# Performance work log

Hardware: AMD Instinct MI355X
Metric: run time of the kernel (lower is better)

## Reference

```python
import jax, jax.numpy as jnp
import numpy as np

B, T, D = 2, 2048, 1024
NH = 16
HD = D // NH


def setup_inputs() -> dict:
    key = jax.random.key(0)
    ks = jax.random.split(key, 5)
    s = 0.02
    return {
        "x": jax.random.normal(ks[0], (B, T, D), dtype=jnp.float32),
        "Wq": jax.random.normal(ks[1], (D, D), dtype=jnp.float32) * s,
        "Wk": jax.random.normal(ks[2], (D, D), dtype=jnp.float32) * s,
        "Wv": jax.random.normal(ks[3], (D, D), dtype=jnp.float32) * s,
        "Wo": jax.random.normal(ks[4], (D, D), dtype=jnp.float32) * s,
        "bo": jnp.zeros((D,), dtype=jnp.float32),
    }


def reference(x, Wq, Wk, Wv, Wo, bo):
    b, t, _ = x.shape
    scale = HD ** -0.5
    # torch Linear: y = x @ W^T
    q = (x @ Wq.T).reshape(b, t, NH, HD)
    k = (x @ Wk.T).reshape(b, t, NH, HD)
    v = (x @ Wv.T).reshape(b, t, NH, HD)
    # scores: [b, nh, t, t]
    s = jnp.einsum("bqhd,bkhd->bhqk", q, k) * scale
    causal = jnp.tril(jnp.ones((t, t), dtype=bool))
    s = jnp.where(causal, s, -jnp.inf)
    p = jax.nn.softmax(s, axis=-1)
    o = jnp.einsum("bhqk,bkhd->bqhd", p, v).reshape(b, t, D)
    return o @ Wo.T + bo
```

## Files before the change

kernel.cpp:

```cpp
#include <hip/hip_runtime.h>


typedef __bf16 bf16x8 __attribute__((ext_vector_type(8)));
typedef float f32x4 __attribute__((ext_vector_type(4)));
typedef unsigned short ushortx8 __attribute__((ext_vector_type(8)));
typedef unsigned short ushortx4 __attribute__((ext_vector_type(4)));

#define T_SEQ 2048
#define NHEAD 16
#define HDIM 64
#define DMODEL 1024

__device__ inline unsigned short f2bf(float f) {
  unsigned int u = __builtin_bit_cast(unsigned int, f);
  unsigned int r = (u + 0x7fffu + ((u >> 16) & 1u)) >> 16;
  return (unsigned short)r;
}

__device__ inline void gl16(const unsigned short* g, unsigned short* l) {
  __builtin_amdgcn_global_load_lds(
      (const __attribute__((address_space(1))) unsigned int*)g,
      (__attribute__((address_space(3))) unsigned int*)l, 16, 0, 0);
}

__global__ void cast_all(const float* __restrict__ x, const float* __restrict__ w0,
                         const float* __restrict__ w1, const float* __restrict__ w2,
                         const float* __restrict__ w3, unsigned short* __restrict__ out) {
  const int NX = 2 * T_SEQ * DMODEL;
  int i = (blockIdx.x * 256 + threadIdx.x) * 4;
  const float* src;
  int off;
  if (i < NX) {
    src = x; off = i;
  } else {
    const int j = i - NX;
    const int sel = j >> 20;
    off = j & ((1 << 20) - 1);
    src = sel == 0 ? w0 : sel == 1 ? w1 : sel == 2 ? w2 : w3;
  }
  float4 v = *reinterpret_cast<const float4*>(src + off);
  ushortx4 o;
  o[0] = f2bf(v.x); o[1] = f2bf(v.y); o[2] = f2bf(v.z); o[3] = f2bf(v.w);
  *reinterpret_cast<ushortx4*>(out + i) = o;
}

__device__ __forceinline__ void gemm_core(
    const unsigned short* __restrict__ A, const unsigned short* __restrict__ Bw,
    int K, int m0, int n0, f32x4 acc[4][4]) {
  __shared__ unsigned short As[4096];
  __shared__ unsigned short Bs[4096];
  const int tid = threadIdx.x;
  const int lane = tid & 63, wid = tid >> 6;
  const int wr = wid >> 1, wc = wid & 1;
  const int lr = lane & 15, lg = lane >> 4;
  const int srow = tid >> 2;
  const int scs = ((tid & 3) ^ (srow & 3)) * 8;
  const unsigned short* ga0 = A + (size_t)(m0 + srow) * K + scs;
  const unsigned short* gb0 = Bw + (size_t)(n0 + srow) * K + scs;
  unsigned short* la0 = As + tid * 8;
  unsigned short* lb0 = Bs + tid * 8;
  const int rca = (lg ^ (lr & 3)) * 8;

  for (int k0 = 0; k0 < K; k0 += 32) {
    __syncthreads();
    gl16(ga0 + k0, la0);
    gl16(ga0 + (size_t)64 * K + k0, la0 + 2048);
    gl16(gb0 + k0, lb0);
    gl16(gb0 + (size_t)64 * K + k0, lb0 + 2048);
    __syncthreads();

    bf16x8 af[4], bfr[4];
#pragma unroll
    for (int t = 0; t < 4; ++t) {
      af[t]  = *reinterpret_cast<const bf16x8*>(&As[(wr * 64 + t * 16 + lr) * 32 + rca]);
      bfr[t] = *reinterpret_cast<const bf16x8*>(&Bs[(wc * 64 + t * 16 + lr) * 32 + rca]);
    }
#pragma unroll
    for (int mi = 0; mi < 4; ++mi)
#pragma unroll
      for (int ni = 0; ni < 4; ++ni)
        acc[mi][ni] = __builtin_amdgcn_mfma_f32_16x16x32_bf16(af[mi], bfr[ni], acc[mi][ni], 0, 0, 0);
  }
}

__device__ __forceinline__ void gemm_core_n64(
    const unsigned short* __restrict__ A, const unsigned short* __restrict__ Bw,
    int K, int m0, int n0, f32x4 acc[4][2]) {
  __shared__ unsigned short As[4096];
  __shared__ unsigned short Bs[2048];
  const int tid = threadIdx.x;
  const int lane = tid & 63, wid = tid >> 6;
  const int wr = wid >> 1, wc = wid & 1;
  const int lr = lane & 15, lg = lane >> 4;
  const int srow = tid >> 2;
  const int scs = ((tid & 3) ^ (srow & 3)) * 8;
  const unsigned short* ga0 = A + (size_t)(m0 + srow) * K + scs;
  const unsigned short* gb0 = Bw + (size_t)(n0 + srow) * K + scs;
  unsigned short* la0 = As + tid * 8;
  unsigned short* lb0 = Bs + tid * 8;
  const int rca = (lg ^ (lr & 3)) * 8;

  for (int k0 = 0; k0 < K; k0 += 32) {
    __syncthreads();
    gl16(ga0 + k0, la0);
    gl16(ga0 + (size_t)64 * K + k0, la0 + 2048);
    gl16(gb0 + k0, lb0);
    __syncthreads();

    bf16x8 af[4], bfr[2];
#pragma unroll
    for (int t = 0; t < 4; ++t)
      af[t] = *reinterpret_cast<const bf16x8*>(&As[(wr * 64 + t * 16 + lr) * 32 + rca]);
#pragma unroll
    for (int t = 0; t < 2; ++t)
      bfr[t] = *reinterpret_cast<const bf16x8*>(&Bs[(wc * 32 + t * 16 + lr) * 32 + rca]);
#pragma unroll
    for (int mi = 0; mi < 4; ++mi)
#pragma unroll
      for (int ni = 0; ni < 2; ++ni)
        acc[mi][ni] = __builtin_amdgcn_mfma_f32_16x16x32_bf16(af[mi], bfr[ni], acc[mi][ni], 0, 0, 0);
  }
}

__global__ __launch_bounds__(256) void gemm_qkv(
    const unsigned short* __restrict__ xb, const unsigned short* __restrict__ Wall,
    unsigned short* __restrict__ Qb, unsigned short* __restrict__ Kb,
    unsigned short* __restrict__ Vtb) {
  const int z = blockIdx.y;
  const int bid = blockIdx.x;
  int m0, n0;
  const unsigned short* A;
  const unsigned short* Bw;
  if (z < 2) {
    n0 = (bid & 7) * 128; m0 = (bid >> 3) * 128;
    A = xb; Bw = Wall + (size_t)z * (DMODEL * DMODEL);
  } else {
    m0 = (bid & 7) * 128; n0 = (bid >> 3) * 128;
    A = Wall + (size_t)2 * (DMODEL * DMODEL); Bw = xb;
  }
  f32x4 acc[4][4] = {};
  gemm_core(A, Bw, DMODEL, m0, n0, acc);

  const int tid = threadIdx.x, lane = tid & 63, wid = tid >> 6;
  const int wr = wid >> 1, wc = wid & 1, lr = lane & 15, lg = lane >> 4;
  const int mb = m0 + wr * 64, nb = n0 + wc * 64;
  const float scale = z == 0 ? 0.125f * 1.44269504089f : 1.0f;
#pragma unroll
  for (int mi = 0; mi < 4; ++mi)
#pragma unroll
    for (int ni = 0; ni < 4; ++ni) {
      const int col = nb + ni * 16 + lr;
#pragma unroll
      for (int j = 0; j < 4; ++j) {
        const int row = mb + mi * 16 + lg * 4 + j;
        const float v = acc[mi][ni][j] * scale;
        if (z < 2) {
          const int b = row >> 11, t = row & (T_SEQ - 1);
          const int h = col >> 6, d = col & (HDIM - 1);
          unsigned short* out = z == 0 ? Qb : Kb;
          out[(((size_t)(b * NHEAD + h) * T_SEQ + t) << 6) + d] = f2bf(v);
        } else {
          const int h = row >> 6, d = row & (HDIM - 1);
          const int b = col >> 11, tt = col & (T_SEQ - 1);
          const int nib = (tt >> 2) & 7;
          const int nib2 = ((nib & 3) << 1) | (nib >> 2);
          const int tp = (tt & ~31) | (nib2 << 2) | (tt & 3);
          Vtb[(((size_t)(b * NHEAD + h) * HDIM + d) << 11) + tp] = f2bf(v);
        }
      }
    }
}

__global__ __launch_bounds__(256) void gemm_proj(
    const unsigned short* __restrict__ Ob, const unsigned short* __restrict__ Wob,
    float* __restrict__ out, const float* __restrict__ bias) {
  const int m0 = blockIdx.y * 128, n0 = blockIdx.x * 64;
  f32x4 acc[4][2] = {};
  gemm_core_n64(Ob, Wob, DMODEL, m0, n0, acc);

  const int tid = threadIdx.x, lane = tid & 63, wid = tid >> 6;
  const int wr = wid >> 1, wc = wid & 1, lr = lane & 15, lg = lane >> 4;
  const int mb = m0 + wr * 64, nb = n0 + wc * 32;
#pragma unroll
  for (int mi = 0; mi < 4; ++mi)
#pragma unroll
    for (int ni = 0; ni < 2; ++ni) {
      const int col = nb + ni * 16 + lr;
      const float bv = bias[col];
#pragma unroll
      for (int j = 0; j < 4; ++j) {
        const int row = mb + mi * 16 + lg * 4 + j;
        out[(size_t)row * DMODEL + col] = acc[mi][ni][j] + bv;
      }
    }
}

__device__ __forceinline__ void attn_step(
    const unsigned short* Kslot, const unsigned short* Vslot,
    const int kh0, const int kh1, const int (&vo)[2],
    const bf16x8 (&qf)[2], f32x4 (&acc)[4], float& mrun, float& lrun,
    const bool domask, const int kb, const int q, const int lg) {
  f32x4 s[4] = {};
  __builtin_amdgcn_s_setprio(1);
#pragma unroll
  for (int c = 0; c < 4; ++c) {
    bf16x8 k0 = *reinterpret_cast<const bf16x8*>(&Kslot[kh0 + c * 1024]);
    bf16x8 k1 = *reinterpret_cast<const bf16x8*>(&Kslot[kh1 + c * 1024]);
    s[c] = __builtin_amdgcn_mfma_f32_16x16x32_bf16(k0, qf[0], s[c], 0, 0, 0);
    s[c] = __builtin_amdgcn_mfma_f32_16x16x32_bf16(k1, qf[1], s[c], 0, 0, 0);
  }
  __builtin_amdgcn_s_setprio(0);
  if (domask) {
#pragma unroll
    for (int c = 0; c < 4; ++c)
#pragma unroll
      for (int j = 0; j < 4; ++j) {
        const int k = kb + c * 16 + lg * 4 + j;
        if (k > q) s[c][j] = -INFINITY;
      }
  }
  float tm = -INFINITY;
#pragma unroll
  for (int c = 0; c < 4; ++c)
#pragma unroll
    for (int j = 0; j < 4; ++j) tm = fmaxf(tm, s[c][j]);
  tm = fmaxf(tm, __shfl_xor(tm, 16, 64));
  tm = fmaxf(tm, __shfl_xor(tm, 32, 64));
  if (!__all(tm <= mrun + 8.f)) {
    const float mnew = fmaxf(mrun, tm);
    const float fac = exp2f(mrun - mnew);
    lrun *= fac;
#pragma unroll
    for (int dt = 0; dt < 4; ++dt)
#pragma unroll
      for (int j = 0; j < 4; ++j) acc[dt][j] *= fac;
    mrun = mnew;
  }
  float tsum = 0.f;
#pragma unroll
  for (int c = 0; c < 4; ++c)
#pragma unroll
    for (int j = 0; j < 4; ++j) {
      const float p = exp2f(s[c][j] - mrun);
      s[c][j] = p;
      tsum += p;
    }
  lrun += tsum;

  bf16x8 pb[2];
#pragma unroll
  for (int ks = 0; ks < 2; ++ks) {
    bf16x8 t8;
#pragma unroll
    for (int e = 0; e < 8; ++e) t8[e] = (__bf16)s[ks * 2 + (e >> 2)][e & 3];
    pb[ks] = t8;
  }
  __builtin_amdgcn_s_setprio(1);
#pragma unroll
  for (int dt = 0; dt < 4; ++dt) {
#pragma unroll
    for (int ks = 0; ks < 2; ++ks) {
      bf16x8 vf = *reinterpret_cast<const bf16x8*>(&Vslot[vo[ks] + dt * 1024]);
      acc[dt] = __builtin_amdgcn_mfma_f32_16x16x32_bf16(vf, pb[ks], acc[dt], 0, 0, 0);
    }
  }
  __builtin_amdgcn_s_setprio(0);
}

__global__ __launch_bounds__(512, 4) void flash_attn(
    const unsigned short* __restrict__ Q, const unsigned short* __restrict__ Kg,
    const unsigned short* __restrict__ Vt, unsigned short* __restrict__ O) {
  __shared__ unsigned short Ks[5][4096];
  __shared__ unsigned short Vs[5][4096];
  const int tid = threadIdx.x, lane = tid & 63, wid = tid >> 6;
  const int lr = lane & 15, lg = lane >> 4, wq = wid & 3;
  const int bid = blockIdx.x;
  const int bh = (bid & 7) * 4 + ((bid >> 3) & 3);
  const int a = (bid >> 5) & 15;
  const int b = 31 - a;
  const bool g0 = wid < 4;
  const int myq1 = g0 ? a : b;
  const int q1 = myq1 * 64 + wq * 16 + lr;
  const int q2 = b * 64 + wq * 16 + lr;
  const size_t base = (size_t)bh * (T_SEQ * HDIM);

  bf16x8 qf1[2], qf2[2];
#pragma unroll
  for (int h = 0; h < 2; ++h) {
    qf1[h] = *reinterpret_cast<const bf16x8*>(Q + base + (size_t)q1 * HDIM + h * 32 + lg * 8);
    qf2[h] = *reinterpret_cast<const bf16x8*>(Q + base + (size_t)q2 * HDIM + h * 32 + lg * 8);
  }

  const int srow = tid >> 3;
  const int schk = ((tid & 7) ^ (srow & 7)) * 8;
  const unsigned short* kst = Kg + base + (size_t)srow * HDIM + schk;
  const unsigned short* vst = Vt + base + (size_t)srow * T_SEQ + schk;

#define STAGE(slot, kt_)                                \
  do {                                                  \
    const int kb_ = (kt_) * 64;                         \
    gl16(kst + (size_t)kb_ * HDIM, &Ks[slot][tid * 8]); \
    gl16(vst + kb_, &Vs[slot][tid * 8]);                \
  } while (0)

  const int kh0 = lr * 64 + ((lg ^ (lr & 7)) * 8);
  const int kh1 = lr * 64 + (((4 + lg) ^ (lr & 7)) * 8);
  int vo[2];
#pragma unroll
  for (int ks = 0; ks < 2; ++ks)
    vo[ks] = lr * 64 + (((ks * 4 + lg) ^ (lr & 7)) * 8);

  float m1 = -INFINITY, l1 = 0.f, m2 = -INFINITY, l2 = 0.f;
  f32x4 acc1[4] = {}, acc2[4] = {};

  STAGE(0, 0);
  STAGE(1, 1);
  asm volatile("s_waitcnt vmcnt(2)" ::: "memory");
  __builtin_amdgcn_s_barrier();
  asm volatile("" ::: "memory");

  int sl = 0;
  for (int kt = 0; kt <= a; ++kt) {
    const int st = kt + 2;
    int sst = sl + 2; if (sst >= 5) sst -= 5;
    if (st <= b) STAGE(sst, st);
    attn_step(Ks[sl], Vs[sl], kh0, kh1, vo, qf1, acc1, m1, l1,
              g0 && (kt == a), kt * 64, q1, lg);
    if (kt < a && st <= b) {
      asm volatile("s_waitcnt vmcnt(2)" ::: "memory");
    } else {
      asm volatile("s_waitcnt vmcnt(0)" ::: "memory");
    }
    __builtin_amdgcn_s_barrier();
    asm volatile("" ::: "memory");
    ++sl; if (sl >= 5) sl -= 5;
  }

  {
    int s3 = sl + 2; if (s3 >= 5) s3 -= 5;
    if (a + 3 <= b) STAGE(s3, a + 3);
  }
  for (int t0 = a + 1; t0 <= b; t0 += 2) {
    int s1 = sl + 1; if (s1 >= 5) s1 -= 5;
    int s3 = sl + 3; if (s3 >= 5) s3 -= 5;
    int s4 = sl + 4; if (s4 >= 5) s4 -= 5;
    if (t0 + 3 <= b) STAGE(s3, t0 + 3);
    if (t0 + 4 <= b) STAGE(s4, t0 + 4);
    if (!g0) {
      attn_step(Ks[sl], Vs[sl], kh0, kh1, vo, qf2, acc1, m1, l1,
                t0 == b, t0 * 64, q2, lg);
    } else if (t0 + 1 <= b) {
      attn_step(Ks[s1], Vs[s1], kh0, kh1, vo, qf2, acc2, m2, l2,
                false, (t0 + 1) * 64, q2, lg);
    }
    if (t0 + 4 <= b) {
      asm volatile("s_waitcnt vmcnt(2)" ::: "memory");
    } else {
      asm volatile("s_waitcnt vmcnt(0)" ::: "memory");
    }
    __builtin_amdgcn_s_barrier();
    asm volatile("" ::: "memory");
    sl += 2; if (sl >= 5) sl -= 5;
  }
#undef STAGE

  float* sm = reinterpret_cast<float*>(&Ks[0][0]);
  const int lid = (wq * 64 + lane) * 18;
  if (g0) {
    float* p = sm + lid;
    p[0] = m2; p[1] = l2;
#pragma unroll
    for (int dt = 0; dt < 4; ++dt)
#pragma unroll
      for (int j = 0; j < 4; ++j) p[2 + dt * 4 + j] = acc2[dt][j];
  }
  __syncthreads();
  if (!g0) {
    const float* p = sm + lid;
    const float mo = p[0], lo = p[1];
    const float ms = fmaxf(m1, mo);
    const float f1 = exp2f(m1 - ms), f2 = exp2f(mo - ms);
    l1 = l1 * f1 + lo * f2;
#pragma unroll
    for (int dt = 0; dt < 4; ++dt)
#pragma unroll
      for (int j = 0; j < 4; ++j)
        acc1[dt][j] = acc1[dt][j] * f1 + p[2 + dt * 4 + j] * f2;
  }

  l1 += __shfl_xor(l1, 16, 64);
  l1 += __shfl_xor(l1, 32, 64);

  const int b_ = bh >> 4, h_ = bh & (NHEAD - 1);
  const float inv = 1.0f / l1;
  unsigned short* orow = O + (((size_t)(b_ * T_SEQ + q1)) << 10) + h_ * HDIM + lg * 4;
#pragma unroll
  for (int dt = 0; dt < 4; ++dt) {
    ushortx4 o4;
#pragma unroll
    for (int j = 0; j < 4; ++j) o4[j] = f2bf(acc1[dt][j] * inv);
    *reinterpret_cast<ushortx4*>(orow + dt * 16) = o4;
  }
}

extern "C" void kernel_launch(void* const* d_in, const int* in_sizes, int n_in,
                              void* d_out, int out_size, void* d_ws, size_t ws_size,
                              hipStream_t stream) {
  const float* x  = (const float*)d_in[0];
  const float* Wq = (const float*)d_in[1];
  const float* Wk = (const float*)d_in[2];
  const float* Wv = (const float*)d_in[3];
  const float* Wo = (const float*)d_in[4];
  const float* bo = (const float*)d_in[5];
  float* out = (float*)d_out;

  const int M = 2 * T_SEQ;
  const int NXD = DMODEL * DMODEL;
  const int NX = M * DMODEL;

  unsigned short* ws = (unsigned short*)d_ws;
  unsigned short* xb  = ws;
  unsigned short* Wqb = xb + NX;
  unsigned short* Wob = Wqb + 3 * (size_t)NXD;
  unsigned short* Qb  = Wqb + 4 * (size_t)NXD;
  unsigned short* Kbf = Qb + NX;
  unsigned short* Vtb = Kbf + NX;
  unsigned short* Ob  = Vtb + NX;

  cast_all<<<(NX + 4 * NXD) / 1024, 256, 0, stream>>>(x, Wq, Wk, Wv, Wo, xb);

  dim3 gq(256, 3);
  gemm_qkv<<<gq, 256, 0, stream>>>(xb, Wqb, Qb, Kbf, Vtb);

  flash_attn<<<512, 512, 0, stream>>>(Qb, Kbf, Vtb, Ob);

  dim3 gg(DMODEL / 64, M / 128);
  gemm_proj<<<gg, 256, 0, stream>>>(Ob, Wob, out, bo);
}
```

Baseline: 104.1 us.

## Have each attention wave process both paired query tiles, sharing K/V fragment loads

The flash-attention block drops from 512 to 256 threads. Each wave now owns 16 rows of both the early query tile and its paired late query tile. During the shared causal prefix, one K/V fragment read from LDS feeds interleaved MFMAs for both query sets, and the tail is split into two independent accumulators that are merged in registers. This removes the end-of-kernel LDS exchange and __syncthreads, and halves LDS fragment reads per MFMA in the shared phase. The cost is higher register pressure, fewer waves per block, and each thread staging twice as many K/V chunks.

```diff
diff --git a/kernel.cpp b/kernel.cpp
--- a/kernel.cpp
+++ b/kernel.cpp
@@ -195,6 +195,44 @@
     }
 }
 
+__device__ __forceinline__ void softmax_pack(
+    f32x4 (&s)[4], f32x4 (&acc)[4], float& mrun, float& lrun, bf16x8 (&pb)[2]) {
+  float tm = -INFINITY;
+#pragma unroll
+  for (int c = 0; c < 4; ++c)
+#pragma unroll
+    for (int j = 0; j < 4; ++j) tm = fmaxf(tm, s[c][j]);
+  tm = fmaxf(tm, __shfl_xor(tm, 16, 64));
+  tm = fmaxf(tm, __shfl_xor(tm, 32, 64));
+  if (!__all(tm <= mrun + 8.f)) {
+    const float mnew = fmaxf(mrun, tm);
+    const float fac = exp2f(mrun - mnew);
+    lrun *= fac;
+#pragma unroll
+    for (int dt = 0; dt < 4; ++dt)
+#pragma unroll
+      for (int j = 0; j < 4; ++j) acc[dt][j] *= fac;
+    mrun = mnew;
+  }
+  float tsum = 0.f;
+#pragma unroll
+  for (int c = 0; c < 4; ++c)
+#pragma unroll
+    for (int j = 0; j < 4; ++j) {
+      const float p = exp2f(s[c][j] - mrun);
+      s[c][j] = p;
+      tsum += p;
+    }
+  lrun += tsum;
+#pragma unroll
+  for (int ks = 0; ks < 2; ++ks) {
+    bf16x8 t8;
+#pragma unroll
+    for (int e = 0; e < 8; ++e) t8[e] = (__bf16)s[ks * 2 + (e >> 2)][e & 3];
+    pb[ks] = t8;
+  }
+}
+
 __device__ __forceinline__ void attn_step(
     const unsigned short* Kslot, const unsigned short* Vslot,
     const int kh0, const int kh1, const int (&vo)[2],
@@ -219,76 +257,85 @@
         if (k > q) s[c][j] = -INFINITY;
       }
   }
-  float tm = -INFINITY;
-#pragma unroll
-  for (int c = 0; c < 4; ++c)
-#pragma unroll
-    for (int j = 0; j < 4; ++j) tm = fmaxf(tm, s[c][j]);
-  tm = fmaxf(tm, __shfl_xor(tm, 16, 64));
-  tm = fmaxf(tm, __shfl_xor(tm, 32, 64));
-  if (!__all(tm <= mrun + 8.f)) {
-    const float mnew = fmaxf(mrun, tm);
-    const float fac = exp2f(mrun - mnew);
-    lrun *= fac;
-#pragma unroll
-    for (int dt = 0; dt < 4; ++dt)
-#pragma unroll
-      for (int j = 0; j < 4; ++j) acc[dt][j] *= fac;
-    mrun = mnew;
-  }
-  float tsum = 0.f;
-#pragma unroll
-  for (int c = 0; c < 4; ++c)
-#pragma unroll
-    for (int j = 0; j < 4; ++j) {
-      const float p = exp2f(s[c][j] - mrun);
-      s[c][j] = p;
-      tsum += p;
-    }
-  lrun += tsum;
-
   bf16x8 pb[2];
-#pragma unroll
-  for (int ks = 0; ks < 2; ++ks) {
-    bf16x8 t8;
-#pragma unroll
-    for (int e = 0; e < 8; ++e) t8[e] = (__bf16)s[ks * 2 + (e >> 2)][e & 3];
-    pb[ks] = t8;
-  }
+  softmax_pack(s, acc, mrun, lrun, pb);
   __builtin_amdgcn_s_setprio(1);
 #pragma unroll
-  for (int dt = 0; dt < 4; ++dt) {
+  for (int dt = 0; dt < 4; ++dt)
 #pragma unroll
     for (int ks = 0; ks < 2; ++ks) {
       bf16x8 vf = *reinterpret_cast<const bf16x8*>(&Vslot[vo[ks] + dt * 1024]);
       acc[dt] = __builtin_amdgcn_mfma_f32_16x16x32_bf16(vf, pb[ks], acc[dt], 0, 0, 0);
     }
-  }
   __builtin_amdgcn_s_setprio(0);
 }
 
-__global__ __launch_bounds__(512, 4) void flash_attn(
+__device__ __forceinline__ void attn_step2(
+    const unsigned short* Kslot, const unsigned short* Vslot,
+    const int kh0, const int kh1, const int (&vo)[2],
+    const bf16x8 (&qfA)[2], f32x4 (&accA)[4], float& mA, float& lA, const bool maskA,
+    const bf16x8 (&qfB)[2], f32x4 (&accB)[4], float& mB, float& lB,
+    const int kb, const int qA, const int lg) {
+  bf16x8 kf[4][2];
+#pragma unroll
+  for (int c = 0; c < 4; ++c) {
+    kf[c][0] = *reinterpret_cast<const bf16x8*>(&Kslot[kh0 + c * 1024]);
+    kf[c][1] = *reinterpret_cast<const bf16x8*>(&Kslot[kh1 + c * 1024]);
+  }
+  f32x4 sA[4] = {}, sB[4] = {};
+  __builtin_amdgcn_s_setprio(1);
+#pragma unroll
+  for (int c = 0; c < 4; ++c) {
+    sA[c] = __builtin_amdgcn_mfma_f32_16x16x32_bf16(kf[c][0], qfA[0], sA[c], 0, 0, 0);
+    sB[c] = __builtin_amdgcn_mfma_f32_16x16x32_bf16(kf[c][0], qfB[0], sB[c], 0, 0, 0);
+    sA[c] = __builtin_amdgcn_mfma_f32_16x16x32_bf16(kf[c][1], qfA[1], sA[c], 0, 0, 0);
+    sB[c] = __builtin_amdgcn_mfma_f32_16x16x32_bf16(kf[c][1], qfB[1], sB[c], 0, 0, 0);
+  }
+  __builtin_amdgcn_s_setprio(0);
+  if (maskA) {
+#pragma unroll
+    for (int c = 0; c < 4; ++c)
+#pragma unroll
+      for (int j = 0; j < 4; ++j) {
+        const int k = kb + c * 16 + lg * 4 + j;
+        if (k > qA) sA[c][j] = -INFINITY;
+      }
+  }
+  bf16x8 pbA[2], pbB[2];
+  softmax_pack(sA, accA, mA, lA, pbA);
+  softmax_pack(sB, accB, mB, lB, pbB);
+  __builtin_amdgcn_s_setprio(1);
+#pragma unroll
+  for (int dt = 0; dt < 4; ++dt)
+#pragma unroll
+    for (int ks = 0; ks < 2; ++ks) {
+      bf16x8 vf = *reinterpret_cast<const bf16x8*>(&Vslot[vo[ks] + dt * 1024]);
+      accA[dt] = __builtin_amdgcn_mfma_f32_16x16x32_bf16(vf, pbA[ks], accA[dt], 0, 0, 0);
+      accB[dt] = __builtin_amdgcn_mfma_f32_16x16x32_bf16(vf, pbB[ks], accB[dt], 0, 0, 0);
+    }
+  __builtin_amdgcn_s_setprio(0);
+}
+
+__global__ __launch_bounds__(256, 2) void flash_attn(
     const unsigned short* __restrict__ Q, const unsigned short* __restrict__ Kg,
     const unsigned short* __restrict__ Vt, unsigned short* __restrict__ O) {
   __shared__ unsigned short Ks[5][4096];
   __shared__ unsigned short Vs[5][4096];
   const int tid = threadIdx.x, lane = tid & 63, wid = tid >> 6;
-  const int lr = lane & 15, lg = lane >> 4, wq = wid & 3;
+  const int lr = lane & 15, lg = lane >> 4;
   const int bid = blockIdx.x;
   const int bh = (bid & 7) * 4 + ((bid >> 3) & 3);
   const int a = (bid >> 5) & 15;
   const int b = 31 - a;
-  const bool g0 = wid < 4;
-  const int myq1 = g0 ? a : b;
-  const int q1 = myq1 * 64 + wq * 16 + lr;
-  const int q2 = b * 64 + wq * 16 + lr;
+  const int qA = a * 64 + wid * 16 + lr;
+  const int qB = b * 64 + wid * 16 + lr;
   const size_t base = (size_t)bh * (T_SEQ * HDIM);
 
-  bf16x8 qf1[2], qf2[2];
+  bf16x8 qfA[2], qfB[2];
 #pragma unroll
   for (int h = 0; h < 2; ++h) {
-    qf1[h] = *reinterpret_cast<const bf16x8*>(Q + base + (size_t)q1 * HDIM + h * 32 + lg * 8);
-    qf2[h] = *reinterpret_cast<const bf16x8*>(Q + base + (size_t)q2 * HDIM + h * 32 + lg * 8);
+    qfA[h] = *reinterpret_cast<const bf16x8*>(Q + base + (size_t)qA * HDIM + h * 32 + lg * 8);
+    qfB[h] = *reinterpret_cast<const bf16x8*>(Q + base + (size_t)qB * HDIM + h * 32 + lg * 8);
   }
 
   const int srow = tid >> 3;
@@ -296,11 +343,13 @@
   const unsigned short* kst = Kg + base + (size_t)srow * HDIM + schk;
   const unsigned short* vst = Vt + base + (size_t)srow * T_SEQ + schk;
 
-#define STAGE(slot, kt_)                                \
-  do {                                                  \
-    const int kb_ = (kt_) * 64;                         \
-    gl16(kst + (size_t)kb_ * HDIM, &Ks[slot][tid * 8]); \
-    gl16(vst + kb_, &Vs[slot][tid * 8]);                \
+#define STAGE(slot, kt_)                                              \
+  do {                                                                \
+    const int kb_ = (kt_) * 64;                                       \
+    gl16(kst + (size_t)kb_ * HDIM, &Ks[slot][tid * 8]);               \
+    gl16(kst + (size_t)(kb_ + 32) * HDIM, &Ks[slot][2048 + tid * 8]); \
+    gl16(vst + kb_, &Vs[slot][tid * 8]);                              \
+    gl16(vst + 32 * T_SEQ + kb_, &Vs[slot][2048 + tid * 8]);          \
   } while (0)
 
   const int kh0 = lr * 64 + ((lg ^ (lr & 7)) * 8);
@@ -310,24 +359,24 @@
   for (int ks = 0; ks < 2; ++ks)
     vo[ks] = lr * 64 + (((ks * 4 + lg) ^ (lr & 7)) * 8);
 
-  float m1 = -INFINITY, l1 = 0.f, m2 = -INFINITY, l2 = 0.f;
-  f32x4 acc1[4] = {}, acc2[4] = {};
+  float mA = -INFINITY, lA = 0.f, mB = -INFINITY, lB = 0.f;
+  f32x4 accA[4] = {}, accB[4] = {};
 
   STAGE(0, 0);
   STAGE(1, 1);
-  asm volatile("s_waitcnt vmcnt(2)" ::: "memory");
+  asm volatile("s_waitcnt vmcnt(4)" ::: "memory");
   __builtin_amdgcn_s_barrier();
   asm volatile("" ::: "memory");
 
   int sl = 0;
   for (int kt = 0; kt <= a; ++kt) {
-    const int st = kt + 2;
     int sst = sl + 2; if (sst >= 5) sst -= 5;
-    if (st <= b) STAGE(sst, st);
-    attn_step(Ks[sl], Vs[sl], kh0, kh1, vo, qf1, acc1, m1, l1,
-              g0 && (kt == a), kt * 64, q1, lg);
-    if (kt < a && st <= b) {
-      asm volatile("s_waitcnt vmcnt(2)" ::: "memory");
+    if (kt + 2 <= b) STAGE(sst, kt + 2);
+    attn_step2(Ks[sl], Vs[sl], kh0, kh1, vo,
+               qfA, accA, mA, lA, (kt == a),
+               qfB, accB, mB, lB, kt * 64, qA, lg);
+    if (kt < a) {
+      asm volatile("s_waitcnt vmcnt(4)" ::: "memory");
     } else {
       asm volatile("s_waitcnt vmcnt(0)" ::: "memory");
     }
@@ -337,24 +386,24 @@
   }
 
   {
-    int s3 = sl + 2; if (s3 >= 5) s3 -= 5;
-    if (a + 3 <= b) STAGE(s3, a + 3);
-  }
+    int sp = sl + 2; if (sp >= 5) sp -= 5;
+    if (a + 3 <= b) STAGE(sp, a + 3);
+  }
+  float m2 = -INFINITY, l2 = 0.f;
+  f32x4 acc2[4] = {};
   for (int t0 = a + 1; t0 <= b; t0 += 2) {
     int s1 = sl + 1; if (s1 >= 5) s1 -= 5;
     int s3 = sl + 3; if (s3 >= 5) s3 -= 5;
     int s4 = sl + 4; if (s4 >= 5) s4 -= 5;
     if (t0 + 3 <= b) STAGE(s3, t0 + 3);
     if (t0 + 4 <= b) STAGE(s4, t0 + 4);
-    if (!g0) {
-      attn_step(Ks[sl], Vs[sl], kh0, kh1, vo, qf2, acc1, m1, l1,
-                t0 == b, t0 * 64, q2, lg);
-    } else if (t0 + 1 <= b) {
-      attn_step(Ks[s1], Vs[s1], kh0, kh1, vo, qf2, acc2, m2, l2,
-                false, (t0 + 1) * 64, q2, lg);
-    }
+    attn_step(Ks[sl], Vs[sl], kh0, kh1, vo, qfB, accB, mB, lB,
+              (t0 == b), t0 * 64, qB, lg);
+    if (t0 + 1 <= b)
+      attn_step(Ks[s1], Vs[s1], kh0, kh1, vo, qfB, acc2, m2, l2,
+                false, (t0 + 1) * 64, qB, lg);
     if (t0 + 4 <= b) {
-      asm volatile("s_waitcnt vmcnt(2)" ::: "memory");
+      asm volatile("s_waitcnt vmcnt(4)" ::: "memory");
     } else {
       asm volatile("s_waitcnt vmcnt(0)" ::: "memory");
     }
@@ -364,42 +413,36 @@
   }
 #undef STAGE
 
-  float* sm = reinterpret_cast<float*>(&Ks[0][0]);
-  const int lid = (wq * 64 + lane) * 18;
-  if (g0) {
-    float* p = sm + lid;
-    p[0] = m2; p[1] = l2;
+  {
+    const float ms = fmaxf(mB, m2);
+    const float f1 = exp2f(mB - ms), f2 = exp2f(m2 - ms);
+    lB = lB * f1 + l2 * f2;
 #pragma unroll
     for (int dt = 0; dt < 4; ++dt)
 #pragma unroll
-      for (int j = 0; j < 4; ++j) p[2 + dt * 4 + j] = acc2[dt][j];
-  }
-  __syncthreads();
-  if (!g0) {
-    const float* p = sm + lid;
-    const float mo = p[0], lo = p[1];
-    const float ms = fmaxf(m1, mo);
-    const float f1 = exp2f(m1 - ms), f2 = exp2f(mo - ms);
-    l1 = l1 * f1 + lo * f2;
-#pragma unroll
-    for (int dt = 0; dt < 4; ++dt)
-#pragma unroll
       for (int j = 0; j < 4; ++j)
-        acc1[dt][j] = acc1[dt][j] * f1 + p[2 + dt * 4 + j] * f2;
-  }
-
-  l1 += __shfl_xor(l1, 16, 64);
-  l1 += __shfl_xor(l1, 32, 64);
+        accB[dt][j] = accB[dt][j] * f1 + acc2[dt][j] * f2;
+  }
+
+  lA += __shfl_xor(lA, 16, 64);
+  lA += __shfl_xor(lA, 32, 64);
+  lB += __shfl_xor(lB, 16, 64);
+  lB += __shfl_xor(lB, 32, 64);
 
   const int b_ = bh >> 4, h_ = bh & (NHEAD - 1);
-  const float inv = 1.0f / l1;
-  unsigned short* orow = O + (((size_t)(b_ * T_SEQ + q1)) << 10) + h_ * HDIM + lg * 4;
+  const float invA = 1.0f / lA, invB = 1.0f / lB;
+  unsigned short* orowA = O + (((size_t)(b_ * T_SEQ + qA)) << 10) + h_ * HDIM + lg * 4;
+  unsigned short* orowB = O + (((size_t)(b_ * T_SEQ + qB)) << 10) + h_ * HDIM + lg * 4;
 #pragma unroll
   for (int dt = 0; dt < 4; ++dt) {
-    ushortx4 o4;
-#pragma unroll
-    for (int j = 0; j < 4; ++j) o4[j] = f2bf(acc1[dt][j] * inv);
-    *reinterpret_cast<ushortx4*>(orow + dt * 16) = o4;
+    ushortx4 oa, ob;
+#pragma unroll
+    for (int j = 0; j < 4; ++j) {
+      oa[j] = f2bf(accA[dt][j] * invA);
+      ob[j] = f2bf(accB[dt][j] * invB);
+    }
+    *reinterpret_cast<ushortx4*>(orowA + dt * 16) = oa;
+    *reinterpret_cast<ushortx4*>(orowB + dt * 16) = ob;
   }
 }
 
@@ -432,7 +475,7 @@
   dim3 gq(256, 3);
   gemm_qkv<<<gq, 256, 0, stream>>>(xb, Wqb, Qb, Kbf, Vtb);
 
-  flash_attn<<<512, 512, 0, stream>>>(Qb, Kbf, Vtb, Ob);
+  flash_attn<<<512, 256, 0, stream>>>(Qb, Kbf, Vtb, Ob);
 
   dim3 gg(DMODEL / 64, M / 128);
   gemm_proj<<<gg, 256, 0, stream>>>(Ob, Wob, out, bo);
```

Result: no change. 105.1 us (+1.0%).
